# Optimization experiments

Measured on AMD Instinct MI355X. Metric: run time of the kernel, lower is better.

## Reference

```python
import jax, jax.numpy as jnp
import numpy as np

ALLOWED_SPANLEN = 7
NEG = -10000.0      # init value for logalpha, matching torch fill_(-10000.)
MASK_NEG = -1e9     # additive mask for out-of-window span starts


def setup_inputs() -> dict:
    key = jax.random.key(0)
    k1, k2 = jax.random.split(key)
    B, L, T = 16, 128, 11  # batch, sent_len, tagset_size (9 tags + START + STOP)
    scores = jax.random.normal(k1, (B, L, L, T, T), dtype=jnp.float32)
    # mask holds sentence lengths in [L//2, L] (used as gather index into logalpha)
    mask = jax.random.randint(k2, (B,), L // 2, L + 1, dtype=jnp.int32)
    return {"scores": scores, "mask": mask}


def reference(scores, mask):
    """Semi-CRF forward DP (get_logloss_denominator).

    scores: (B, L, L, T, T) -- scores[b, j, i, y_prev, y] is the score of a span
            [j, i] labeled y, with previous segment label y_prev.
    mask:   (B,) sentence lengths.
    """
    B, L, _, T, _ = scores.shape
    K = ALLOWED_SPANLEN
    start_id, stop_id = T - 1, T - 2

    alpha0 = jnp.full((B, L + 1, T), NEG, dtype=scores.dtype)
    alpha0 = alpha0.at[:, 0, start_id].set(0.0)

    # Re-index scores by span-end position so scan can stream one end per step.
    scores_by_end = jnp.moveaxis(scores, 2, 0)  # (L_end, B, L_start, T, T)
    offs = jnp.arange(K)

    def step(alpha, xs):
        i, sc = xs                # i in [1..L]; sc: (B, L, Tprev, Tcur), end = i-1
        js = i - K + offs         # candidate span starts: [i-K, i-1]
        valid = (js >= 0)[None, :, None, None]
        jsc = jnp.clip(js, 0, L - 1)
        a_w = jnp.take(alpha, jsc, axis=1)   # (B, K, Tprev)
        s_w = jnp.take(sc, jsc, axis=1)      # (B, K, Tprev, Tcur)
        t = jnp.where(valid, s_w + a_w[:, :, :, None], MASK_NEG)
        new = jax.nn.logsumexp(t, axis=(1, 2))           # (B, Tcur)
        alpha = jax.lax.dynamic_update_slice(alpha, new[:, None, :], (0, i, 0))
        return alpha, None

    alpha, _ = jax.lax.scan(step, alpha0, (jnp.arange(1, L + 1), scores_by_end))
    # gather logalpha at the sentence-length position for each batch element
    final = alpha[jnp.arange(B), mask, :]                # (B, T)
    return final[:, stop_id].sum()
```

## Files before the change

### kernel.cpp

```cpp
#include <hip/hip_runtime.h>
#include <math.h>

#define LL 128
#define TT 11
#define NP 121
#define KK 7
#define GS 20
#define SPW 240
#define NSLOT 8
#define PANEF 1024

#define LOG2E 1.4426950408889634f
#define LN2   0.6931471805599453f

__device__ __forceinline__ float fast_exp2(float x) { return __builtin_amdgcn_exp2f(x); }
__device__ __forceinline__ float fast_log2(float x) { return __builtin_amdgcn_logf(x); }
#if __has_builtin(__builtin_amdgcn_rcpf)
__device__ __forceinline__ float fast_rcp(float x) { return __builtin_amdgcn_rcpf(x); }
#else
__device__ __forceinline__ float fast_rcp(float x) { return 1.0f / x; }
#endif
__device__ __forceinline__ float rfl(float x) {
    return __int_as_float(__builtin_amdgcn_readfirstlane(__float_as_int(x)));
}
__device__ __forceinline__ void cfence() { __builtin_amdgcn_wave_barrier(); }
#define VMWAIT28() asm volatile("s_waitcnt vmcnt(28)" ::: "memory")
#define VMWAIT0()  asm volatile("s_waitcnt vmcnt(0)"  ::: "memory")
#define LGKM0()    asm volatile("s_waitcnt lgkmcnt(0)" ::: "memory")

__device__ __forceinline__ void block_sync() {
    asm volatile("" ::: "memory");
    __builtin_amdgcn_s_barrier();
    asm volatile("" ::: "memory");
}

__global__ __launch_bounds__(192, 1) void hscrf_pc3(const float* __restrict__ scores,
                                                    const int* __restrict__ mask,
                                                    float* __restrict__ out,
                                                    int n_batch)
{
    const int tid = threadIdx.x;
    const int l   = tid & 63;
    const int wid = tid >> 6;
    const int b   = blockIdx.x;
    if (b >= n_batch) return;

    __shared__ __align__(64) float ring[NSLOT][PANEF];
    __shared__ __align__(64) float sp[SPW];

    const float* sb = scores + (size_t)b * (size_t)(LL * (size_t)LL * NP);

    const int o1  = l + 64;
    const bool val1 = (o1 < NP);
    const int o1c = val1 ? o1 : 0;

    if (wid >= 1) {
        const int pw = wid - 1;

        float Xa0[KK], Xa1[KK], Xb0[KK], Xb1[KK];
        float Ya0[KK], Ya1[KK], Yb0[KK], Yb1[KK];

        auto issue_pane = [&](int p, float (&a0)[KK], float (&a1)[KK]) {
#pragma unroll
            for (int k = 0; k < KK; ++k) {
                const int j = p - KK + k; const int jc = j < 0 ? 0 : j;
                const float* sl = sb + ((size_t)jc * LL + (size_t)(p - 1)) * NP;
                a0[k] = sl[l];
                a1[k] = sl[o1c];
            }
        };
        auto issue_pair = [&](int base, float (&a0)[KK], float (&a1)[KK],
                              float (&b0)[KK], float (&b1)[KK]) {
            issue_pane(base,     a0, a1);
            issue_pane(base + 2, b0, b1);
        };

        auto conv1 = [&](int p, const float (&a0)[KK], const float (&a1)[KK]) {
            const int slot = p & (NSLOT - 1);
            float v0[8], w1[8];
#pragma unroll
            for (int k = 0; k < KK; ++k) {
                const bool ok = (p - KK + k) >= 0;
                const float t0 = fast_exp2(a0[k] * LOG2E);
                const float t1 = fast_exp2(a1[k] * LOG2E);
                v0[k] = ok ? t0 : 0.0f;
                w1[k] = (ok && val1) ? t1 : 0.0f;
            }
            v0[7] = 0.0f; w1[7] = 0.0f;
            float4* dst = (float4*)&ring[slot][0];
            dst[l]       = make_float4(v0[0], v0[1], v0[2], v0[3]);
            dst[128 + l] = make_float4(v0[4], v0[5], v0[6], v0[7]);
            dst[64 + l]  = make_float4(w1[0], w1[1], w1[2], w1[3]);
            dst[192 + l] = make_float4(w1[4], w1[5], w1[6], w1[7]);
        };
        auto conv_pair = [&](int base, const float (&a0)[KK], const float (&a1)[KK],
                             const float (&b0)[KK], const float (&b1)[KK]) {
            conv1(base,     a0, a1);
            conv1(base + 2, b0, b1);
        };

        issue_pair(1 + pw, Xa0, Xa1, Xb0, Xb1);
        VMWAIT0();
        conv_pair(1 + pw, Xa0, Xa1, Xb0, Xb1);
        issue_pair(5 + pw, Xa0, Xa1, Xb0, Xb1);
        LGKM0(); block_sync();

        for (int t = 1; t <= 29; t += 2) {
            issue_pair(4 * t + 5 + pw, Ya0, Ya1, Yb0, Yb1);
            VMWAIT28();
            conv_pair(4 * t + 1 + pw, Xa0, Xa1, Xb0, Xb1);
            LGKM0(); block_sync();

            issue_pair(4 * t + 9 + pw, Xa0, Xa1, Xb0, Xb1);
            VMWAIT28();
            conv_pair(4 * t + 5 + pw, Ya0, Ya1, Yb0, Yb1);
            LGKM0(); block_sync();
        }
        VMWAIT0();
        conv_pair(125 + pw, Xa0, Xa1, Xb0, Xb1);
        LGKM0(); block_sync();
    } else {
        const int y0 = l % TT,   yp0 = l / TT;
        const int y1 = o1c % TT, yp1 = o1c / TT;
        const int i0w = y0 * GS + yp0;
        const int i1w = val1 ? (y1 * GS + yp1) : (220 + (l - 57));

        if (l < TT) sp[l * GS + 11] = 0.0f;

        const int mb = mask[b];

        float W0[KK], W1[KK];
#pragma unroll
        for (int k = 0; k < KK; ++k) { W0[k] = 0.0f; W1[k] = 0.0f; }
        W0[KK - 1] = (yp0 == TT - 1) ? 1.0f : 0.0f;
        W1[KK - 1] = (val1 && yp1 == TT - 1) ? 1.0f : 0.0f;

        float Cc = 0.0f;
        float savedS = 1.0f;
        float savedC = 0.0f;

        __builtin_amdgcn_s_setprio(1);
        block_sync();

        auto body = [&](int i, const float4& ea0, const float4& ea1,
                               const float4& eb0, const float4& eb1) {
            float p0 = fmaf(ea0.x, W0[0], ea0.y * W0[1]);
            float q0 = fmaf(ea0.z, W0[2], ea0.w * W0[3]);
            float u0 = fmaf(ea1.x, W0[4], ea1.y * W0[5]);
            float s0 = (p0 + q0) + fmaf(ea1.z, W0[6], u0);
            float p1 = fmaf(eb0.x, W1[0], eb0.y * W1[1]);
            float q1 = fmaf(eb0.z, W1[2], eb0.w * W1[3]);
            float u1 = fmaf(eb1.x, W1[4], eb1.y * W1[5]);
            float s1 = (p1 + q1) + fmaf(eb1.z, W1[6], u1);
            sp[i0w] = s0;
            sp[i1w] = s1;

            cfence();

            const float4 qa0 = *(const float4*)(sp + yp0 * GS);
            const float4 qb0 = *(const float4*)(sp + yp0 * GS + 4);
            const float4 qc0 = *(const float4*)(sp + yp0 * GS + 8);
            const float4 qa1 = *(const float4*)(sp + yp1 * GS);
            const float4 qb1 = *(const float4*)(sp + yp1 * GS + 4);
            const float4 qc1 = *(const float4*)(sp + yp1 * GS + 8);

            const float SA = (((qa0.x + qa0.y) + (qa0.z + qa0.w)) +
                              ((qb0.x + qb0.y) + (qb0.z + qb0.w))) +
                             ((qc0.x + qc0.y) + (qc0.z + qc0.w));
            const float SB = (((qa1.x + qa1.y) + (qa1.z + qa1.w)) +
                              ((qb1.x + qb1.y) + (qb1.z + qb1.w))) +
                             ((qc1.x + qc1.y) + (qc1.z + qc1.w));

            const float s0u = rfl(SA);
            const float r = fast_rcp(s0u);

            savedS = (i == mb) ? SB : savedS;
            savedC = (i == mb) ? Cc : savedC;
            Cc += fast_log2(s0u);

#pragma unroll
            for (int k = 0; k < KK - 1; ++k) { W0[k] = W0[k + 1] * r; W1[k] = W1[k + 1] * r; }
            W0[KK - 1] = SA * r;
            W1[KK - 1] = SB * r;

            cfence();
        };

        for (int t = 1; t <= 32; ++t) {
            const int p0 = 4 * t - 3;

            const float4* r0 = (const float4*)&ring[p0 & (NSLOT - 1)][0];
            const float4* r1 = (const float4*)&ring[(p0 + 1) & (NSLOT - 1)][0];
            const float4 Aa0 = r0[l], Aa1 = r0[128 + l];
            const float4 Ab0 = r0[64 + l], Ab1 = r0[192 + l];
            const float4 Ba0 = r1[l], Ba1 = r1[128 + l];
            const float4 Bb0 = r1[64 + l], Bb1 = r1[192 + l];

            body(p0, Aa0, Aa1, Ab0, Ab1);

            const float4* r2 = (const float4*)&ring[(p0 + 2) & (NSLOT - 1)][0];
            const float4* r3 = (const float4*)&ring[(p0 + 3) & (NSLOT - 1)][0];
            const float4 Ca0 = r2[l], Ca1 = r2[128 + l];
            const float4 Cb0 = r2[64 + l], Cb1 = r2[192 + l];
            const float4 Da0 = r3[l], Da1 = r3[128 + l];
            const float4 Db0 = r3[64 + l], Db1 = r3[192 + l];

            body(p0 + 1, Ba0, Ba1, Bb0, Bb1);
            body(p0 + 2, Ca0, Ca1, Cb0, Cb1);
            body(p0 + 3, Da0, Da1, Db0, Db1);

            if (t < 32) block_sync();
        }

        if (l == 35) {
            atomicAdd(out, (savedC + fast_log2(savedS)) * LN2);
        }
    }
}

extern "C" void kernel_launch(void* const* d_in, const int* in_sizes, int n_in,
                              void* d_out, int out_size, void* d_ws, size_t ws_size,
                              hipStream_t stream) {
    const float* scores = (const float*)d_in[0];
    const int*   mask   = (const int*)d_in[1];
    float* out = (float*)d_out;
    const int B = in_sizes[1];

    hipMemsetAsync(out, 0, sizeof(float) * out_size, stream);

    (void)d_ws; (void)ws_size;

    hscrf_pc3<<<B, 192, 0, stream>>>(scores, mask, out, B);
}
```

Before: 177.6 us.

## Remap tag pairs to 16-lane rows and reduce via shuffles instead of LDS

```diff
diff --git a/kernel.cpp b/kernel.cpp
--- a/kernel.cpp
+++ b/kernel.cpp
@@ -5,10 +5,8 @@
 #define TT 11
 #define NP 121
 #define KK 7
-#define GS 20
-#define SPW 240
 #define NSLOT 8
-#define PANEF 1024
+#define PANEF 1536
 
 #define LOG2E 1.4426950408889634f
 #define LN2   0.6931471805599453f
@@ -24,7 +22,8 @@
     return __int_as_float(__builtin_amdgcn_readfirstlane(__float_as_int(x)));
 }
 __device__ __forceinline__ void cfence() { __builtin_amdgcn_wave_barrier(); }
-#define VMWAIT28() asm volatile("s_waitcnt vmcnt(28)" ::: "memory")
+#define VMWAIT42() asm volatile("s_waitcnt vmcnt(42)" ::: "memory")
+#define VMWAIT21() asm volatile("s_waitcnt vmcnt(21)" ::: "memory")
 #define VMWAIT0()  asm volatile("s_waitcnt vmcnt(0)"  ::: "memory")
 #define LGKM0()    asm volatile("s_waitcnt lgkmcnt(0)" ::: "memory")
 
@@ -34,7 +33,7 @@
     asm volatile("" ::: "memory");
 }
 
-__global__ __launch_bounds__(192, 1) void hscrf_pc3(const float* __restrict__ scores,
+__global__ __launch_bounds__(192, 1) void hscrf_pc4(const float* __restrict__ scores,
                                                     const int* __restrict__ mask,
                                                     float* __restrict__ out,
                                                     int n_batch)
@@ -46,173 +45,170 @@
     if (b >= n_batch) return;
 
     __shared__ __align__(64) float ring[NSLOT][PANEF];
-    __shared__ __align__(64) float sp[SPW];
 
     const float* sb = scores + (size_t)b * (size_t)(LL * (size_t)LL * NP);
 
-    const int o1  = l + 64;
-    const bool val1 = (o1 < NP);
-    const int o1c = val1 ? o1 : 0;
+    const int r = l >> 4;
+    const int c = l & 15;
 
     if (wid >= 1) {
         const int pw = wid - 1;
 
-        float Xa0[KK], Xa1[KK], Xb0[KK], Xb1[KK];
-        float Ya0[KK], Ya1[KK], Yb0[KK], Yb1[KK];
-
-        auto issue_pane = [&](int p, float (&a0)[KK], float (&a1)[KK]) {
+        const bool vy  = (c <= 10);
+        const bool vm2 = vy && (r <= 2);
+        const int off0 = vy  ? (r * TT + c)       : 0;
+        const int off1 = vy  ? ((r + 4) * TT + c) : 0;
+        const int off2 = vm2 ? ((r + 8) * TT + c) : 0;
+
+        float A[3][KK], B[3][KK], C[3][KK], D[3][KK];
+
+        auto issueP = [&](int p, float (&g)[3][KK]) {
 #pragma unroll
             for (int k = 0; k < KK; ++k) {
                 const int j = p - KK + k; const int jc = j < 0 ? 0 : j;
                 const float* sl = sb + ((size_t)jc * LL + (size_t)(p - 1)) * NP;
-                a0[k] = sl[l];
-                a1[k] = sl[o1c];
+                g[0][k] = sl[off0];
+                g[1][k] = sl[off1];
+                g[2][k] = sl[off2];
             }
         };
-        auto issue_pair = [&](int base, float (&a0)[KK], float (&a1)[KK],
-                              float (&b0)[KK], float (&b1)[KK]) {
-            issue_pane(base,     a0, a1);
-            issue_pane(base + 2, b0, b1);
-        };
-
-        auto conv1 = [&](int p, const float (&a0)[KK], const float (&a1)[KK]) {
+
+        auto convP = [&](int p, const float (&g)[3][KK]) {
             const int slot = p & (NSLOT - 1);
-            float v0[8], w1[8];
+            float4* b16 = (float4*)&ring[slot][0];
+            float e0[KK], e1[KK], e2[KK];
 #pragma unroll
             for (int k = 0; k < KK; ++k) {
-                const bool ok = (p - KK + k) >= 0;
-                const float t0 = fast_exp2(a0[k] * LOG2E);
-                const float t1 = fast_exp2(a1[k] * LOG2E);
-                v0[k] = ok ? t0 : 0.0f;
-                w1[k] = (ok && val1) ? t1 : 0.0f;
+                const bool okj = (p - KK + k) >= 0;
+                const float t0 = fast_exp2(g[0][k] * LOG2E);
+                const float t1 = fast_exp2(g[1][k] * LOG2E);
+                const float t2 = fast_exp2(g[2][k] * LOG2E);
+                e0[k] = (okj && vy)  ? t0 : 0.0f;
+                e1[k] = (okj && vy)  ? t1 : 0.0f;
+                e2[k] = (okj && vm2) ? t2 : 0.0f;
             }
-            v0[7] = 0.0f; w1[7] = 0.0f;
-            float4* dst = (float4*)&ring[slot][0];
-            dst[l]       = make_float4(v0[0], v0[1], v0[2], v0[3]);
-            dst[128 + l] = make_float4(v0[4], v0[5], v0[6], v0[7]);
-            dst[64 + l]  = make_float4(w1[0], w1[1], w1[2], w1[3]);
-            dst[192 + l] = make_float4(w1[4], w1[5], w1[6], w1[7]);
-        };
-        auto conv_pair = [&](int base, const float (&a0)[KK], const float (&a1)[KK],
-                             const float (&b0)[KK], const float (&b1)[KK]) {
-            conv1(base,     a0, a1);
-            conv1(base + 2, b0, b1);
-        };
-
-        issue_pair(1 + pw, Xa0, Xa1, Xb0, Xb1);
-        VMWAIT0();
-        conv_pair(1 + pw, Xa0, Xa1, Xb0, Xb1);
-        issue_pair(5 + pw, Xa0, Xa1, Xb0, Xb1);
+            b16[l]             = make_float4(e0[0], e0[1], e0[2], e0[3]);
+            b16[192 + l]       = make_float4(e0[4], e0[5], e0[6], 0.0f);
+            b16[64 + l]        = make_float4(e1[0], e1[1], e1[2], e1[3]);
+            b16[256 + l]       = make_float4(e1[4], e1[5], e1[6], 0.0f);
+            b16[128 + l]       = make_float4(e2[0], e2[1], e2[2], e2[3]);
+            b16[320 + l]       = make_float4(e2[4], e2[5], e2[6], 0.0f);
+        };
+
+        issueP(1 + pw, A);
+        issueP(3 + pw, B);
+        VMWAIT21();
+        convP(1 + pw, A);
+        issueP(5 + pw, C);
+        VMWAIT21();
+        convP(3 + pw, B);
+        issueP(7 + pw, D);
         LGKM0(); block_sync();
 
         for (int t = 1; t <= 29; t += 2) {
-            issue_pair(4 * t + 5 + pw, Ya0, Ya1, Yb0, Yb1);
-            VMWAIT28();
-            conv_pair(4 * t + 1 + pw, Xa0, Xa1, Xb0, Xb1);
+            issueP(4 * t + 5 + pw, A);
+            VMWAIT42();
+            convP(4 * t + 1 + pw, C);
+            issueP(4 * t + 7 + pw, B);
+            VMWAIT42();
+            convP(4 * t + 3 + pw, D);
             LGKM0(); block_sync();
-
-            issue_pair(4 * t + 9 + pw, Xa0, Xa1, Xb0, Xb1);
-            VMWAIT28();
-            conv_pair(4 * t + 5 + pw, Ya0, Ya1, Yb0, Yb1);
+            issueP(4 * t + 9 + pw, C);
+            VMWAIT42();
+            convP(4 * t + 5 + pw, A);
+            issueP(4 * t + 11 + pw, D);
+            VMWAIT42();
+            convP(4 * t + 7 + pw, B);
             LGKM0(); block_sync();
         }
+        VMWAIT21();
+        convP(125 + pw, C);
         VMWAIT0();
-        conv_pair(125 + pw, Xa0, Xa1, Xb0, Xb1);
+        convP(127 + pw, D);
         LGKM0(); block_sync();
     } else {
-        const int y0 = l % TT,   yp0 = l / TT;
-        const int y1 = o1c % TT, yp1 = o1c / TT;
-        const int i0w = y0 * GS + yp0;
-        const int i1w = val1 ? (y1 * GS + yp1) : (220 + (l - 57));
-
-        if (l < TT) sp[l * GS + 11] = 0.0f;
-
         const int mb = mask[b];
-
-        float W0[KK], W1[KK];
-#pragma unroll
-        for (int k = 0; k < KK; ++k) { W0[k] = 0.0f; W1[k] = 0.0f; }
-        W0[KK - 1] = (yp0 == TT - 1) ? 1.0f : 0.0f;
-        W1[KK - 1] = (val1 && yp1 == TT - 1) ? 1.0f : 0.0f;
+        const int r1s = r + 4, r2s = r + 8;
+
+        float W0[KK], W1[KK], W2[KK];
+#pragma unroll
+        for (int k = 0; k < KK; ++k) { W0[k] = 0.0f; W1[k] = 0.0f; W2[k] = 0.0f; }
+        W0[KK - 1] = (r     == 10) ? 1.0f : 0.0f;
+        W1[KK - 1] = (r + 4 == 10) ? 1.0f : 0.0f;
+        W2[KK - 1] = (r + 8 == 10) ? 1.0f : 0.0f;
 
         float Cc = 0.0f;
-        float savedS = 1.0f;
-        float savedC = 0.0f;
+        float savedS = 1.0f, savedC = 0.0f;
+
+        struct F6 { float4 a0, a1, b0, b1, c0, c1; };
+        F6 EA, EB, EC;
+
+        auto readPane = [&](int p, F6& d) {
+            const float4* b16 = (const float4*)&ring[p & (NSLOT - 1)][0];
+            d.a0 = b16[l];        d.a1 = b16[192 + l];
+            d.b0 = b16[64 + l];   d.b1 = b16[256 + l];
+            d.c0 = b16[128 + l];  d.c1 = b16[320 + l];
+        };
+
+        auto step = [&](int i, const F6& E, F6* pf, int pfp) {
+            float u0 = fmaf(E.a0.x, W0[0], E.a0.y * W0[1]);
+            float v0 = fmaf(E.a0.z, W0[2], E.a0.w * W0[3]);
+            float w0 = fmaf(E.a1.x, W0[4], E.a1.y * W0[5]);
+            float s0 = (u0 + v0) + fmaf(E.a1.z, W0[6], w0);
+            float u1 = fmaf(E.b0.x, W1[0], E.b0.y * W1[1]);
+            float v1 = fmaf(E.b0.z, W1[2], E.b0.w * W1[3]);
+            float w1 = fmaf(E.b1.x, W1[4], E.b1.y * W1[5]);
+            float s1 = (u1 + v1) + fmaf(E.b1.z, W1[6], w1);
+            float u2 = fmaf(E.c0.x, W2[0], E.c0.y * W2[1]);
+            float v2 = fmaf(E.c0.z, W2[2], E.c0.w * W2[3]);
+            float w2 = fmaf(E.c1.x, W2[4], E.c1.y * W2[5]);
+            float s2 = (u2 + v2) + fmaf(E.c1.z, W2[6], w2);
+
+            float t = (s0 + s1) + s2;
+            t += __shfl_xor(t, 16);
+            t += __shfl_xor(t, 32);
+
+            const float n0 = __shfl(t, r);
+            const float n1 = __shfl(t, r1s);
+            const float n2 = __shfl(t, r2s);
+
+            cfence();
+            if (pf) readPane(pfp, *pf);
+            cfence();
+
+            const float s0u = rfl(t);
+            const float rr = fast_rcp(s0u);
+
+            savedS = (i == mb) ? t  : savedS;
+            savedC = (i == mb) ? Cc : savedC;
+            Cc += fast_log2(s0u);
+
+#pragma unroll
+            for (int k = 0; k < KK - 1; ++k) {
+                W0[k] = W0[k + 1] * rr;
+                W1[k] = W1[k + 1] * rr;
+                W2[k] = W2[k + 1] * rr;
+            }
+            W0[KK - 1] = n0 * rr;
+            W1[KK - 1] = n1 * rr;
+            W2[KK - 1] = n2 * rr;
+        };
 
         __builtin_amdgcn_s_setprio(1);
         block_sync();
 
-        auto body = [&](int i, const float4& ea0, const float4& ea1,
-                               const float4& eb0, const float4& eb1) {
-            float p0 = fmaf(ea0.x, W0[0], ea0.y * W0[1]);
-            float q0 = fmaf(ea0.z, W0[2], ea0.w * W0[3]);
-            float u0 = fmaf(ea1.x, W0[4], ea1.y * W0[5]);
-            float s0 = (p0 + q0) + fmaf(ea1.z, W0[6], u0);
-            float p1 = fmaf(eb0.x, W1[0], eb0.y * W1[1]);
-            float q1 = fmaf(eb0.z, W1[2], eb0.w * W1[3]);
-            float u1 = fmaf(eb1.x, W1[4], eb1.y * W1[5]);
-            float s1 = (p1 + q1) + fmaf(eb1.z, W1[6], u1);
-            sp[i0w] = s0;
-            sp[i1w] = s1;
-
-            cfence();
-
-            const float4 qa0 = *(const float4*)(sp + yp0 * GS);
-            const float4 qb0 = *(const float4*)(sp + yp0 * GS + 4);
-            const float4 qc0 = *(const float4*)(sp + yp0 * GS + 8);
-            const float4 qa1 = *(const float4*)(sp + yp1 * GS);
-            const float4 qb1 = *(const float4*)(sp + yp1 * GS + 4);
-            const float4 qc1 = *(const float4*)(sp + yp1 * GS + 8);
-
-            const float SA = (((qa0.x + qa0.y) + (qa0.z + qa0.w)) +
-                              ((qb0.x + qb0.y) + (qb0.z + qb0.w))) +
-                             ((qc0.x + qc0.y) + (qc0.z + qc0.w));
-            const float SB = (((qa1.x + qa1.y) + (qa1.z + qa1.w)) +
-                              ((qb1.x + qb1.y) + (qb1.z + qb1.w))) +
-                             ((qc1.x + qc1.y) + (qc1.z + qc1.w));
-
-            const float s0u = rfl(SA);
-            const float r = fast_rcp(s0u);
-
-            savedS = (i == mb) ? SB : savedS;
-            savedC = (i == mb) ? Cc : savedC;
-            Cc += fast_log2(s0u);
-
-#pragma unroll
-            for (int k = 0; k < KK - 1; ++k) { W0[k] = W0[k + 1] * r; W1[k] = W1[k + 1] * r; }
-            W0[KK - 1] = SA * r;
-            W1[KK - 1] = SB * r;
-
-            cfence();
-        };
-
         for (int t = 1; t <= 32; ++t) {
             const int p0 = 4 * t - 3;
-
-            const float4* r0 = (const float4*)&ring[p0 & (NSLOT - 1)][0];
-            const float4* r1 = (const float4*)&ring[(p0 + 1) & (NSLOT - 1)][0];
-            const float4 Aa0 = r0[l], Aa1 = r0[128 + l];
-            const float4 Ab0 = r0[64 + l], Ab1 = r0[192 + l];
-            const float4 Ba0 = r1[l], Ba1 = r1[128 + l];
-            const float4 Bb0 = r1[64 + l], Bb1 = r1[192 + l];
-
-            body(p0, Aa0, Aa1, Ab0, Ab1);
-
-            const float4* r2 = (const float4*)&ring[(p0 + 2) & (NSLOT - 1)][0];
-            const float4* r3 = (const float4*)&ring[(p0 + 3) & (NSLOT - 1)][0];
-            const float4 Ca0 = r2[l], Ca1 = r2[128 + l];
-            const float4 Cb0 = r2[64 + l], Cb1 = r2[192 + l];
-            const float4 Da0 = r3[l], Da1 = r3[128 + l];
-            const float4 Db0 = r3[64 + l], Db1 = r3[192 + l];
-
-            body(p0 + 1, Ba0, Ba1, Bb0, Bb1);
-            body(p0 + 2, Ca0, Ca1, Cb0, Cb1);
-            body(p0 + 3, Da0, Da1, Db0, Db1);
-
+            readPane(p0, EA);
+            readPane(p0 + 1, EB);
+            step(p0,     EA, &EC, p0 + 2);
+            step(p0 + 1, EB, &EA, p0 + 3);
+            step(p0 + 2, EC, nullptr, 0);
+            step(p0 + 3, EA, nullptr, 0);
             if (t < 32) block_sync();
         }
 
-        if (l == 35) {
+        if (l == 9) {
             atomicAdd(out, (savedC + fast_log2(savedS)) * LN2);
         }
     }
@@ -230,5 +226,5 @@
 
     (void)d_ws; (void)ws_size;
 
-    hscrf_pc3<<<B, 192, 0, stream>>>(scores, mask, out, B);
-}
+    hscrf_pc4<<<B, 192, 0, stream>>>(scores, mask, out, B);
+}
```

New measurement: 184.3 us. 3.8% more time.

## Process two batch elements per block with one shared compute wave

Applied to the files above, without the earlier changes.

```diff
diff --git a/kernel.cpp b/kernel.cpp
--- a/kernel.cpp
+++ b/kernel.cpp
@@ -34,7 +34,7 @@
     asm volatile("" ::: "memory");
 }
 
-__global__ __launch_bounds__(192, 1) void hscrf_pc3(const float* __restrict__ scores,
+__global__ __launch_bounds__(320, 1) void hscrf_pc5(const float* __restrict__ scores,
                                                     const int* __restrict__ mask,
                                                     float* __restrict__ out,
                                                     int n_batch)
@@ -42,20 +42,25 @@
     const int tid = threadIdx.x;
     const int l   = tid & 63;
     const int wid = tid >> 6;
-    const int b   = blockIdx.x;
-    if (b >= n_batch) return;
-
-    __shared__ __align__(64) float ring[NSLOT][PANEF];
-    __shared__ __align__(64) float sp[SPW];
-
-    const float* sb = scores + (size_t)b * (size_t)(LL * (size_t)LL * NP);
+    const int blk = blockIdx.x;
+
+    __shared__ __align__(64) float ring[2][NSLOT][PANEF];
+    __shared__ __align__(64) float sp[2][SPW];
+
+    const int bA = 2 * blk;
+    const int bB = 2 * blk + 1;
+    if (bA >= n_batch) return;
 
     const int o1  = l + 64;
     const bool val1 = (o1 < NP);
     const int o1c = val1 ? o1 : 0;
 
     if (wid >= 1) {
-        const int pw = wid - 1;
+        const int bi = (wid - 1) >> 1;
+        const int pw = (wid - 1) & 1;
+        const int bb = (2 * blk + bi < n_batch) ? (2 * blk + bi) : bA;
+        const float* sb = scores + (size_t)bb * (size_t)(LL * (size_t)LL * NP);
+        float (*myring)[PANEF] = ring[bi];
 
         float Xa0[KK], Xa1[KK], Xb0[KK], Xb1[KK];
         float Ya0[KK], Ya1[KK], Yb0[KK], Yb1[KK];
@@ -87,7 +92,7 @@
                 w1[k] = (ok && val1) ? t1 : 0.0f;
             }
             v0[7] = 0.0f; w1[7] = 0.0f;
-            float4* dst = (float4*)&ring[slot][0];
+            float4* dst = (float4*)&myring[slot][0];
             dst[l]       = make_float4(v0[0], v0[1], v0[2], v0[3]);
             dst[128 + l] = make_float4(v0[4], v0[5], v0[6], v0[7]);
             dst[64 + l]  = make_float4(w1[0], w1[1], w1[2], w1[3]);
@@ -125,95 +130,133 @@
         const int i0w = y0 * GS + yp0;
         const int i1w = val1 ? (y1 * GS + yp1) : (220 + (l - 57));
 
-        if (l < TT) sp[l * GS + 11] = 0.0f;
-
-        const int mb = mask[b];
-
-        float W0[KK], W1[KK];
-#pragma unroll
-        for (int k = 0; k < KK; ++k) { W0[k] = 0.0f; W1[k] = 0.0f; }
-        W0[KK - 1] = (yp0 == TT - 1) ? 1.0f : 0.0f;
-        W1[KK - 1] = (val1 && yp1 == TT - 1) ? 1.0f : 0.0f;
-
-        float Cc = 0.0f;
-        float savedS = 1.0f;
-        float savedC = 0.0f;
+        float* spA = sp[0];
+        float* spB = sp[1];
+        if (l < TT) { spA[l * GS + 11] = 0.0f; spB[l * GS + 11] = 0.0f; }
+
+        const int mbA = mask[bA];
+        const int mbB = (bB < n_batch) ? mask[bB] : mask[bA];
+
+        float WA0[KK], WA1[KK], WB0[KK], WB1[KK];
+#pragma unroll
+        for (int k = 0; k < KK; ++k) { WA0[k] = 0.0f; WA1[k] = 0.0f;
+                                       WB0[k] = 0.0f; WB1[k] = 0.0f; }
+        const float w0init = (yp0 == TT - 1) ? 1.0f : 0.0f;
+        const float w1init = (val1 && yp1 == TT - 1) ? 1.0f : 0.0f;
+        WA0[KK - 1] = w0init; WA1[KK - 1] = w1init;
+        WB0[KK - 1] = w0init; WB1[KK - 1] = w1init;
+
+        float CcA = 0.0f, CcB = 0.0f;
+        float savedSA = 1.0f, savedCA = 0.0f;
+        float savedSB = 1.0f, savedCB = 0.0f;
+
+        struct E4 { float4 a0, a1, b0, b1; };
+        E4 A_EA, A_EB, A_EC, B_EA, B_EB, B_EC;
+
+        auto readPane = [&](const float (*rg)[PANEF], int p, E4& d) {
+            const float4* b16 = (const float4*)&rg[p & (NSLOT - 1)][0];
+            d.a0 = b16[l];      d.a1 = b16[128 + l];
+            d.b0 = b16[64 + l]; d.b1 = b16[192 + l];
+        };
+
+        auto body2 = [&](int i, const E4& EA, const E4& EB) {
+            float p0a = fmaf(EA.a0.x, WA0[0], EA.a0.y * WA0[1]);
+            float q0a = fmaf(EA.a0.z, WA0[2], EA.a0.w * WA0[3]);
+            float u0a = fmaf(EA.a1.x, WA0[4], EA.a1.y * WA0[5]);
+            float s0a = (p0a + q0a) + fmaf(EA.a1.z, WA0[6], u0a);
+            float p1a = fmaf(EA.b0.x, WA1[0], EA.b0.y * WA1[1]);
+            float q1a = fmaf(EA.b0.z, WA1[2], EA.b0.w * WA1[3]);
+            float u1a = fmaf(EA.b1.x, WA1[4], EA.b1.y * WA1[5]);
+            float s1a = (p1a + q1a) + fmaf(EA.b1.z, WA1[6], u1a);
+            spA[i0w] = s0a;
+            spA[i1w] = s1a;
+            float p0b = fmaf(EB.a0.x, WB0[0], EB.a0.y * WB0[1]);
+            float q0b = fmaf(EB.a0.z, WB0[2], EB.a0.w * WB0[3]);
+            float u0b = fmaf(EB.a1.x, WB0[4], EB.a1.y * WB0[5]);
+            float s0b = (p0b + q0b) + fmaf(EB.a1.z, WB0[6], u0b);
+            float p1b = fmaf(EB.b0.x, WB1[0], EB.b0.y * WB1[1]);
+            float q1b = fmaf(EB.b0.z, WB1[2], EB.b0.w * WB1[3]);
+            float u1b = fmaf(EB.b1.x, WB1[4], EB.b1.y * WB1[5]);
+            float s1b = (p1b + q1b) + fmaf(EB.b1.z, WB1[6], u1b);
+            spB[i0w] = s0b;
+            spB[i1w] = s1b;
+
+            cfence();
+
+            const float4 qa0A = *(const float4*)(spA + yp0 * GS);
+            const float4 qb0A = *(const float4*)(spA + yp0 * GS + 4);
+            const float4 qc0A = *(const float4*)(spA + yp0 * GS + 8);
+            const float4 qa1A = *(const float4*)(spA + yp1 * GS);
+            const float4 qb1A = *(const float4*)(spA + yp1 * GS + 4);
+            const float4 qc1A = *(const float4*)(spA + yp1 * GS + 8);
+            const float4 qa0B = *(const float4*)(spB + yp0 * GS);
+            const float4 qb0B = *(const float4*)(spB + yp0 * GS + 4);
+            const float4 qc0B = *(const float4*)(spB + yp0 * GS + 8);
+            const float4 qa1B = *(const float4*)(spB + yp1 * GS);
+            const float4 qb1B = *(const float4*)(spB + yp1 * GS + 4);
+            const float4 qc1B = *(const float4*)(spB + yp1 * GS + 8);
+
+            const float SAA = (((qa0A.x + qa0A.y) + (qa0A.z + qa0A.w)) +
+                               ((qb0A.x + qb0A.y) + (qb0A.z + qb0A.w))) +
+                              ((qc0A.x + qc0A.y) + (qc0A.z + qc0A.w));
+            const float SBA = (((qa1A.x + qa1A.y) + (qa1A.z + qa1A.w)) +
+                               ((qb1A.x + qb1A.y) + (qb1A.z + qb1A.w))) +
+                              ((qc1A.x + qc1A.y) + (qc1A.z + qc1A.w));
+            const float SAB = (((qa0B.x + qa0B.y) + (qa0B.z + qa0B.w)) +
+                               ((qb0B.x + qb0B.y) + (qb0B.z + qb0B.w))) +
+                              ((qc0B.x + qc0B.y) + (qc0B.z + qc0B.w));
+            const float SBB = (((qa1B.x + qa1B.y) + (qa1B.z + qa1B.w)) +
+                               ((qb1B.x + qb1B.y) + (qb1B.z + qb1B.w))) +
+                              ((qc1B.x + qc1B.y) + (qc1B.z + qc1B.w));
+
+            const float s0uA = rfl(SAA);
+            const float rA = fast_rcp(s0uA);
+            const float s0uB = rfl(SAB);
+            const float rB = fast_rcp(s0uB);
+
+            savedSA = (i == mbA) ? SBA : savedSA;
+            savedCA = (i == mbA) ? CcA : savedCA;
+            savedSB = (i == mbB) ? SBB : savedSB;
+            savedCB = (i == mbB) ? CcB : savedCB;
+            CcA += fast_log2(s0uA);
+            CcB += fast_log2(s0uB);
+
+#pragma unroll
+            for (int k = 0; k < KK - 1; ++k) {
+                WA0[k] = WA0[k + 1] * rA; WA1[k] = WA1[k + 1] * rA;
+                WB0[k] = WB0[k + 1] * rB; WB1[k] = WB1[k + 1] * rB;
+            }
+            WA0[KK - 1] = SAA * rA; WA1[KK - 1] = SBA * rA;
+            WB0[KK - 1] = SAB * rB; WB1[KK - 1] = SBB * rB;
+
+            cfence();
+        };
 
         __builtin_amdgcn_s_setprio(1);
         block_sync();
 
-        auto body = [&](int i, const float4& ea0, const float4& ea1,
-                               const float4& eb0, const float4& eb1) {
-            float p0 = fmaf(ea0.x, W0[0], ea0.y * W0[1]);
-            float q0 = fmaf(ea0.z, W0[2], ea0.w * W0[3]);
-            float u0 = fmaf(ea1.x, W0[4], ea1.y * W0[5]);
-            float s0 = (p0 + q0) + fmaf(ea1.z, W0[6], u0);
-            float p1 = fmaf(eb0.x, W1[0], eb0.y * W1[1]);
-            float q1 = fmaf(eb0.z, W1[2], eb0.w * W1[3]);
-            float u1 = fmaf(eb1.x, W1[4], eb1.y * W1[5]);
-            float s1 = (p1 + q1) + fmaf(eb1.z, W1[6], u1);
-            sp[i0w] = s0;
-            sp[i1w] = s1;
-
-            cfence();
-
-            const float4 qa0 = *(const float4*)(sp + yp0 * GS);
-            const float4 qb0 = *(const float4*)(sp + yp0 * GS + 4);
-            const float4 qc0 = *(const float4*)(sp + yp0 * GS + 8);
-            const float4 qa1 = *(const float4*)(sp + yp1 * GS);
-            const float4 qb1 = *(const float4*)(sp + yp1 * GS + 4);
-            const float4 qc1 = *(const float4*)(sp + yp1 * GS + 8);
-
-            const float SA = (((qa0.x + qa0.y) + (qa0.z + qa0.w)) +
-                              ((qb0.x + qb0.y) + (qb0.z + qb0.w))) +
-                             ((qc0.x + qc0.y) + (qc0.z + qc0.w));
-            const float SB = (((qa1.x + qa1.y) + (qa1.z + qa1.w)) +
-                              ((qb1.x + qb1.y) + (qb1.z + qb1.w))) +
-                             ((qc1.x + qc1.y) + (qc1.z + qc1.w));
-
-            const float s0u = rfl(SA);
-            const float r = fast_rcp(s0u);
-
-            savedS = (i == mb) ? SB : savedS;
-            savedC = (i == mb) ? Cc : savedC;
-            Cc += fast_log2(s0u);
-
-#pragma unroll
-            for (int k = 0; k < KK - 1; ++k) { W0[k] = W0[k + 1] * r; W1[k] = W1[k + 1] * r; }
-            W0[KK - 1] = SA * r;
-            W1[KK - 1] = SB * r;
-
-            cfence();
-        };
-
         for (int t = 1; t <= 32; ++t) {
             const int p0 = 4 * t - 3;
 
-            const float4* r0 = (const float4*)&ring[p0 & (NSLOT - 1)][0];
-            const float4* r1 = (const float4*)&ring[(p0 + 1) & (NSLOT - 1)][0];
-            const float4 Aa0 = r0[l], Aa1 = r0[128 + l];
-            const float4 Ab0 = r0[64 + l], Ab1 = r0[192 + l];
-            const float4 Ba0 = r1[l], Ba1 = r1[128 + l];
-            const float4 Bb0 = r1[64 + l], Bb1 = r1[192 + l];
-
-            body(p0, Aa0, Aa1, Ab0, Ab1);
-
-            const float4* r2 = (const float4*)&ring[(p0 + 2) & (NSLOT - 1)][0];
-            const float4* r3 = (const float4*)&ring[(p0 + 3) & (NSLOT - 1)][0];
-            const float4 Ca0 = r2[l], Ca1 = r2[128 + l];
-            const float4 Cb0 = r2[64 + l], Cb1 = r2[192 + l];
-            const float4 Da0 = r3[l], Da1 = r3[128 + l];
-            const float4 Db0 = r3[64 + l], Db1 = r3[192 + l];
-
-            body(p0 + 1, Ba0, Ba1, Bb0, Bb1);
-            body(p0 + 2, Ca0, Ca1, Cb0, Cb1);
-            body(p0 + 3, Da0, Da1, Db0, Db1);
+            readPane(ring[0], p0, A_EA);     readPane(ring[1], p0, B_EA);
+            readPane(ring[0], p0 + 1, A_EB); readPane(ring[1], p0 + 1, B_EB);
+
+            body2(p0, A_EA, B_EA);
+
+            readPane(ring[0], p0 + 2, A_EC); readPane(ring[1], p0 + 2, B_EC);
+            readPane(ring[0], p0 + 3, A_EA); readPane(ring[1], p0 + 3, B_EA);
+
+            body2(p0 + 1, A_EB, B_EB);
+            body2(p0 + 2, A_EC, B_EC);
+            body2(p0 + 3, A_EA, B_EA);
 
             if (t < 32) block_sync();
         }
 
         if (l == 35) {
-            atomicAdd(out, (savedC + fast_log2(savedS)) * LN2);
+            atomicAdd(out, (savedCA + fast_log2(savedSA)) * LN2);
+            if (bB < n_batch)
+                atomicAdd(out, (savedCB + fast_log2(savedSB)) * LN2);
         }
     }
 }
@@ -230,5 +273,5 @@
 
     (void)d_ws; (void)ws_size;
 
-    hscrf_pc3<<<B, 192, 0, stream>>>(scores, mask, out, B);
-}
+    hscrf_pc5<<<(B + 1) / 2, 320, 0, stream>>>(scores, mask, out, B);
+}
```

Result: slower. 201.5 us (+13.5%).

## Double ring depth and process eight panes per barrier with rotating LDS prefetch

Applied to the files above, without the earlier changes.

```diff
diff --git a/kernel.cpp b/kernel.cpp
--- a/kernel.cpp
+++ b/kernel.cpp
@@ -7,7 +7,7 @@
 #define KK 7
 #define GS 20
 #define SPW 240
-#define NSLOT 8
+#define NSLOT 16
 #define PANEF 1024
 
 #define LOG2E 1.4426950408889634f
@@ -34,7 +34,7 @@
     asm volatile("" ::: "memory");
 }
 
-__global__ __launch_bounds__(192, 1) void hscrf_pc3(const float* __restrict__ scores,
+__global__ __launch_bounds__(192, 1) void hscrf_pc6(const float* __restrict__ scores,
                                                     const int* __restrict__ mask,
                                                     float* __restrict__ out,
                                                     int n_batch)
@@ -57,8 +57,8 @@
     if (wid >= 1) {
         const int pw = wid - 1;
 
-        float Xa0[KK], Xa1[KK], Xb0[KK], Xb1[KK];
-        float Ya0[KK], Ya1[KK], Yb0[KK], Yb1[KK];
+        float Pa0[KK], Pa1[KK], Pb0[KK], Pb1[KK];
+        float Pc0[KK], Pc1[KK], Pd0[KK], Pd1[KK];
 
         auto issue_pane = [&](int p, float (&a0)[KK], float (&a1)[KK]) {
 #pragma unroll
@@ -68,11 +68,6 @@
                 a0[k] = sl[l];
                 a1[k] = sl[o1c];
             }
-        };
-        auto issue_pair = [&](int base, float (&a0)[KK], float (&a1)[KK],
-                              float (&b0)[KK], float (&b1)[KK]) {
-            issue_pane(base,     a0, a1);
-            issue_pane(base + 2, b0, b1);
         };
 
         auto conv1 = [&](int p, const float (&a0)[KK], const float (&a1)[KK]) {
@@ -93,31 +88,33 @@
             dst[64 + l]  = make_float4(w1[0], w1[1], w1[2], w1[3]);
             dst[192 + l] = make_float4(w1[4], w1[5], w1[6], w1[7]);
         };
-        auto conv_pair = [&](int base, const float (&a0)[KK], const float (&a1)[KK],
-                             const float (&b0)[KK], const float (&b1)[KK]) {
-            conv1(base,     a0, a1);
-            conv1(base + 2, b0, b1);
-        };
-
-        issue_pair(1 + pw, Xa0, Xa1, Xb0, Xb1);
-        VMWAIT0();
-        conv_pair(1 + pw, Xa0, Xa1, Xb0, Xb1);
-        issue_pair(5 + pw, Xa0, Xa1, Xb0, Xb1);
+
+        issue_pane(1 + pw, Pa0, Pa1); issue_pane(3 + pw, Pb0, Pb1);
+        issue_pane(5 + pw, Pc0, Pc1); issue_pane(7 + pw, Pd0, Pd1);
+        VMWAIT28();
+        conv1(1 + pw, Pa0, Pa1); conv1(3 + pw, Pb0, Pb1);
+        issue_pane(9 + pw, Pa0, Pa1); issue_pane(11 + pw, Pb0, Pb1);
+        VMWAIT28();
+        conv1(5 + pw, Pc0, Pc1); conv1(7 + pw, Pd0, Pd1);
+        issue_pane(13 + pw, Pc0, Pc1); issue_pane(15 + pw, Pd0, Pd1);
         LGKM0(); block_sync();
 
-        for (int t = 1; t <= 29; t += 2) {
-            issue_pair(4 * t + 5 + pw, Ya0, Ya1, Yb0, Yb1);
+        for (int t = 1; t <= 14; ++t) {
+            const int base = 8 * t;
             VMWAIT28();
-            conv_pair(4 * t + 1 + pw, Xa0, Xa1, Xb0, Xb1);
-            LGKM0(); block_sync();
-
-            issue_pair(4 * t + 9 + pw, Xa0, Xa1, Xb0, Xb1);
+            conv1(base + 1 + pw, Pa0, Pa1); conv1(base + 3 + pw, Pb0, Pb1);
+            issue_pane(base + 9 + pw, Pa0, Pa1);
+            issue_pane(base + 11 + pw, Pb0, Pb1);
             VMWAIT28();
-            conv_pair(4 * t + 5 + pw, Ya0, Ya1, Yb0, Yb1);
+            conv1(base + 5 + pw, Pc0, Pc1); conv1(base + 7 + pw, Pd0, Pd1);
+            issue_pane(base + 13 + pw, Pc0, Pc1);
+            issue_pane(base + 15 + pw, Pd0, Pd1);
             LGKM0(); block_sync();
         }
+        VMWAIT28();
+        conv1(121 + pw, Pa0, Pa1); conv1(123 + pw, Pb0, Pb1);
         VMWAIT0();
-        conv_pair(125 + pw, Xa0, Xa1, Xb0, Xb1);
+        conv1(125 + pw, Pc0, Pc1); conv1(127 + pw, Pd0, Pd1);
         LGKM0(); block_sync();
     } else {
         const int y0 = l % TT,   yp0 = l / TT;
@@ -139,19 +136,24 @@
         float savedS = 1.0f;
         float savedC = 0.0f;
 
-        __builtin_amdgcn_s_setprio(1);
-        block_sync();
-
-        auto body = [&](int i, const float4& ea0, const float4& ea1,
-                               const float4& eb0, const float4& eb1) {
-            float p0 = fmaf(ea0.x, W0[0], ea0.y * W0[1]);
-            float q0 = fmaf(ea0.z, W0[2], ea0.w * W0[3]);
-            float u0 = fmaf(ea1.x, W0[4], ea1.y * W0[5]);
-            float s0 = (p0 + q0) + fmaf(ea1.z, W0[6], u0);
-            float p1 = fmaf(eb0.x, W1[0], eb0.y * W1[1]);
-            float q1 = fmaf(eb0.z, W1[2], eb0.w * W1[3]);
-            float u1 = fmaf(eb1.x, W1[4], eb1.y * W1[5]);
-            float s1 = (p1 + q1) + fmaf(eb1.z, W1[6], u1);
+        struct E4 { float4 a0, a1, b0, b1; };
+        E4 EA, EB, EC;
+
+        auto readPane = [&](int p, E4& d) {
+            const float4* b16 = (const float4*)&ring[p & (NSLOT - 1)][0];
+            d.a0 = b16[l];      d.a1 = b16[128 + l];
+            d.b0 = b16[64 + l]; d.b1 = b16[192 + l];
+        };
+
+        auto body = [&](int i, const E4& E) {
+            float p0 = fmaf(E.a0.x, W0[0], E.a0.y * W0[1]);
+            float q0 = fmaf(E.a0.z, W0[2], E.a0.w * W0[3]);
+            float u0 = fmaf(E.a1.x, W0[4], E.a1.y * W0[5]);
+            float s0 = (p0 + q0) + fmaf(E.a1.z, W0[6], u0);
+            float p1 = fmaf(E.b0.x, W1[0], E.b0.y * W1[1]);
+            float q1 = fmaf(E.b0.z, W1[2], E.b0.w * W1[3]);
+            float u1 = fmaf(E.b1.x, W1[4], E.b1.y * W1[5]);
+            float s1 = (p1 + q1) + fmaf(E.b1.z, W1[6], u1);
             sp[i0w] = s0;
             sp[i1w] = s1;
 
@@ -186,30 +188,24 @@
             cfence();
         };
 
-        for (int t = 1; t <= 32; ++t) {
-            const int p0 = 4 * t - 3;
-
-            const float4* r0 = (const float4*)&ring[p0 & (NSLOT - 1)][0];
-            const float4* r1 = (const float4*)&ring[(p0 + 1) & (NSLOT - 1)][0];
-            const float4 Aa0 = r0[l], Aa1 = r0[128 + l];
-            const float4 Ab0 = r0[64 + l], Ab1 = r0[192 + l];
-            const float4 Ba0 = r1[l], Ba1 = r1[128 + l];
-            const float4 Bb0 = r1[64 + l], Bb1 = r1[192 + l];
-
-            body(p0, Aa0, Aa1, Ab0, Ab1);
-
-            const float4* r2 = (const float4*)&ring[(p0 + 2) & (NSLOT - 1)][0];
-            const float4* r3 = (const float4*)&ring[(p0 + 3) & (NSLOT - 1)][0];
-            const float4 Ca0 = r2[l], Ca1 = r2[128 + l];
-            const float4 Cb0 = r2[64 + l], Cb1 = r2[192 + l];
-            const float4 Da0 = r3[l], Da1 = r3[128 + l];
-            const float4 Db0 = r3[64 + l], Db1 = r3[192 + l];
-
-            body(p0 + 1, Ba0, Ba1, Bb0, Bb1);
-            body(p0 + 2, Ca0, Ca1, Cb0, Cb1);
-            body(p0 + 3, Da0, Da1, Db0, Db1);
-
-            if (t < 32) block_sync();
+        __builtin_amdgcn_s_setprio(1);
+        block_sync();
+
+        for (int t = 1; t <= 16; ++t) {
+            const int p0 = 8 * t - 7;
+
+            readPane(p0, EA);
+            readPane(p0 + 1, EB);
+            body(p0,     EA); readPane(p0 + 2, EC);
+            body(p0 + 1, EB); readPane(p0 + 3, EA);
+            body(p0 + 2, EC); readPane(p0 + 4, EB);
+            body(p0 + 3, EA); readPane(p0 + 5, EC);
+            body(p0 + 4, EB); readPane(p0 + 6, EA);
+            body(p0 + 5, EC); readPane(p0 + 7, EB);
+            body(p0 + 6, EA);
+            body(p0 + 7, EB);
+
+            if (t < 16) block_sync();
         }
 
         if (l == 35) {
@@ -230,5 +226,5 @@
 
     (void)d_ws; (void)ws_size;
 
-    hscrf_pc3<<<B, 192, 0, stream>>>(scores, mask, out, B);
-}
+    hscrf_pc6<<<B, 192, 0, stream>>>(scores, mask, out, B);
+}
```

Measured after the change: 179.7 us. No clear change (+1.2%).
